# Optimization experiments

Hardware: AMD Instinct MI355X
Metric: run time of the kernel (lower is better)

## Reference

```python
import jax, jax.numpy as jnp
import numpy as np

B, S, D = 2, 2048, 2048
H, KV, HD = 32, 8, 64          # n_heads, n_kv_heads, head_dim
REP = H // KV                  # 4
THETA = 10000.0


def _rotate_half(u):
    h = u.shape[-1] // 2
    return jnp.concatenate([-u[..., h:], u[..., :h]], axis=-1)


def setup_inputs() -> dict:
    key = jax.random.key(0)
    ks = jax.random.split(key, 5)
    x = jax.random.normal(ks[0], (B, S, D), dtype=jnp.float32)
    Wq = jax.random.normal(ks[1], (D, H * HD), dtype=jnp.float32) * 0.02
    Wk = jax.random.normal(ks[2], (D, KV * HD), dtype=jnp.float32) * 0.02
    Wv = jax.random.normal(ks[3], (D, KV * HD), dtype=jnp.float32) * 0.02
    Wo = jax.random.normal(ks[4], (H * HD, D), dtype=jnp.float32) * 0.02
    return {"x": x, "Wq": Wq, "Wk": Wk, "Wv": Wv, "Wo": Wo}


def reference(x, Wq, Wk, Wv, Wo):
    b, s, d = x.shape
    # QKV projections (nn.Linear, no bias)
    q = (x @ Wq).reshape(b, s, H, HD).transpose(0, 2, 1, 3)   # [B,H,S,HD]
    k = (x @ Wk).reshape(b, s, KV, HD).transpose(0, 2, 1, 3)  # [B,KV,S,HD]
    v = (x @ Wv).reshape(b, s, KV, HD).transpose(0, 2, 1, 3)  # [B,KV,S,HD]

    # RoPE (position_offset = 0)
    inv_freq = 1.0 / (THETA ** (jnp.arange(0, HD, 2, dtype=jnp.float32) / HD))
    freqs = jnp.outer(jnp.arange(s, dtype=jnp.float32), inv_freq)  # [S,HD/2]
    emb = jnp.concatenate([freqs, freqs], axis=-1)                  # [S,HD]
    cos, sin = jnp.cos(emb), jnp.sin(emb)
    q = q * cos + _rotate_half(q) * sin
    k = k * cos + _rotate_half(k) * sin

    # Grouped attention: avoid materializing repeated KV tensors.
    qg = q.reshape(b, KV, REP, s, HD)                               # [B,KV,REP,S,HD]
    scale = 1.0 / np.sqrt(HD)
    scores = jnp.einsum('bgrqd,bgkd->bgrqk', qg, k) * scale         # [B,KV,REP,S,S]
    causal = jnp.tril(jnp.ones((s, s), dtype=bool))
    scores = jnp.where(causal, scores, jnp.finfo(jnp.float32).min)
    probs = jax.nn.softmax(scores.astype(jnp.float32), axis=-1).astype(q.dtype)
    out = jnp.einsum('bgrqk,bgkd->bgrqd', probs, v)                 # [B,KV,REP,S,HD]
    out = out.reshape(b, H, s, HD).transpose(0, 2, 1, 3).reshape(b, s, H * HD)
    return out @ Wo                                                  # [B,S,D]
```

## Files before the change

### kernel.cpp

```cpp
#include <hip/hip_runtime.h>
#include <math.h>

typedef __bf16 bf16_t;
typedef bf16_t bf16x8 __attribute__((ext_vector_type(8)));
typedef bf16_t bf16x4 __attribute__((ext_vector_type(4)));
typedef float floatx4 __attribute__((ext_vector_type(4)));
typedef short short4v __attribute__((ext_vector_type(4)));

#define MFMA16(a, b, c) __builtin_amdgcn_mfma_f32_16x16x32_bf16((a), (b), (c), 0, 0, 0)

#if __has_builtin(__builtin_amdgcn_exp2f)
#define PEXP(x) __builtin_amdgcn_exp2f(x)
#define SCORE_SCALE (0.125f * 1.4426950408889634f)
#else
#define PEXP(x) __expf(x)
#define SCORE_SCALE 0.125f
#endif

#if __has_builtin(__builtin_amdgcn_mfma_f32_16x16x16bf16_1k)
#define HAVE_MFMA_K16 1
__device__ __forceinline__ floatx4 mfma_k16(bf16x4 a, bf16x4 b, floatx4 c)
{
    union { bf16x4 v; short4v s; } ua, ub;
    ua.v = a; ub.v = b;
    return __builtin_amdgcn_mfma_f32_16x16x16bf16_1k(ua.s, ub.s, c, 0, 0, 0);
}
#endif

union PU { unsigned u[2]; bf16x4 v; };
union BU { unsigned u[4]; bf16x8 v; };

__device__ __forceinline__ void gld16(const void* g, void* lds)
{
    __builtin_amdgcn_global_load_lds(
        reinterpret_cast<const __attribute__((address_space(1))) void*>(
            reinterpret_cast<uintptr_t>(g)),
        reinterpret_cast<__attribute__((address_space(3))) void*>(
            (unsigned int)reinterpret_cast<uintptr_t>(lds)),
        16, 0, 0);
}

template <int RND>
__device__ __forceinline__ void stageT(
    const bf16_t* __restrict__ g, int K, int r0, int k0,
    bf16_t* lds, int tid, int wave)
{
    #pragma unroll
    for (int i = 0; i < RND; ++i) {
        int c = i * 512 + tid, r = c >> 3, s = c & 7;
        gld16(g + (size_t)(r0 + r) * K + k0 + ((s ^ (r & 7)) << 3),
              lds + (size_t)(i * 512 + wave * 64) * 8);
    }
}

template <typename TC, int BN>
__device__ __forceinline__ void gemm256_body(
    const bf16_t* __restrict__ A, const bf16_t* __restrict__ Bt,
    TC* __restrict__ C, int row0, int col0, int N, int K, bf16_t* smem)
{
    constexpr int NT = BN / 64;
    constexpr int NH = NT / 2;
    constexpr int RB = BN / 64;

    const int tid  = threadIdx.x;
    const int wave = tid >> 6, lane = tid & 63;
    const int quad = lane >> 4, l16 = lane & 15;
    const int wm = (wave >> 2) * 128;
    const int wn = (wave & 3) * (BN / 4);

    bf16_t* As0 = smem;
    bf16_t* As1 = smem + 256 * 64;
    bf16_t* Bs0 = smem + 2 * 256 * 64;
    bf16_t* Bs1 = Bs0 + BN * 64;

    const int ntile = K >> 6;

    floatx4 acc[8][NT] = {};

    stageT<4>(A, K, row0, 0, As0, tid, wave);
    stageT<RB>(Bt, K, col0, 0, Bs0, tid, wave);
    stageT<4>(A, K, row0, 64, As1, tid, wave);

    #pragma unroll 1
    for (int u = 0; u < ntile; ++u) {
        const int d = u & 1;
        bf16_t* Asd = d ? As1 : As0;
        bf16_t* Bsd = d ? Bs1 : Bs0;

        if (u + 1 < ntile)
            __asm__ volatile("s_waitcnt vmcnt(4)" ::: "memory");
        else
            __asm__ volatile("s_waitcnt vmcnt(0)" ::: "memory");
        __builtin_amdgcn_s_barrier();
        __asm__ volatile("" ::: "memory");

        if (u + 1 < ntile)
            stageT<RB>(Bt, K, col0, (u + 1) << 6, d ? Bs0 : Bs1, tid, wave);

        bf16x8 af[8][2], bfr[NH][2];
        #pragma unroll
        for (int mt = 0; mt < 8; ++mt)
            #pragma unroll
            for (int kh = 0; kh < 2; ++kh) {
                int ar = wm + mt * 16 + l16;
                af[mt][kh] = *(const bf16x8*)&Asd[ar * 64 +
                    (((kh * 4 + quad) ^ (ar & 7)) << 3)];
            }
        #pragma unroll
        for (int j = 0; j < NH; ++j)
            #pragma unroll
            for (int kh = 0; kh < 2; ++kh) {
                int br = wn + j * 16 + l16;
                bfr[j][kh] = *(const bf16x8*)&Bsd[br * 64 +
                    (((kh * 4 + quad) ^ (br & 7)) << 3)];
            }

        __builtin_amdgcn_s_setprio(1);
        #pragma unroll
        for (int kh = 0; kh < 2; ++kh)
            #pragma unroll
            for (int mt = 0; mt < 8; ++mt)
                #pragma unroll
                for (int j = 0; j < NH; ++j)
                    acc[mt][j] = MFMA16(af[mt][kh], bfr[j][kh], acc[mt][j]);
        __builtin_amdgcn_s_setprio(0);

        __asm__ volatile("s_waitcnt lgkmcnt(0)" ::: "memory");
        __builtin_amdgcn_s_barrier();
        __asm__ volatile("" ::: "memory");

        if (u + 2 < ntile)
            stageT<4>(A, K, row0, (u + 2) << 6, Asd, tid, wave);

        bf16x8 bf1[NH][2];
        #pragma unroll
        for (int j = 0; j < NH; ++j)
            #pragma unroll
            for (int kh = 0; kh < 2; ++kh) {
                int br = wn + (NH + j) * 16 + l16;
                bf1[j][kh] = *(const bf16x8*)&Bsd[br * 64 +
                    (((kh * 4 + quad) ^ (br & 7)) << 3)];
            }

        __builtin_amdgcn_s_setprio(1);
        #pragma unroll
        for (int kh = 0; kh < 2; ++kh)
            #pragma unroll
            for (int mt = 0; mt < 8; ++mt)
                #pragma unroll
                for (int j = 0; j < NH; ++j)
                    acc[mt][NH + j] = MFMA16(af[mt][kh], bf1[j][kh],
                                             acc[mt][NH + j]);
        __builtin_amdgcn_s_setprio(0);
    }

    #pragma unroll
    for (int mt = 0; mt < 8; ++mt)
        #pragma unroll
        for (int nt = 0; nt < NT; ++nt)
            #pragma unroll
            for (int r = 0; r < 4; ++r)
                C[(size_t)(row0 + wm + mt * 16 + quad * 4 + r) * N
                  + col0 + wn + nt * 16 + l16] = (TC)acc[mt][nt][r];
}

__global__ __launch_bounds__(512, 2) void gemm256_qkv(
    const bf16_t* __restrict__ A, const bf16_t* __restrict__ BtQ,
    const bf16_t* __restrict__ BtK, const bf16_t* __restrict__ BtV,
    bf16_t* __restrict__ CQ, bf16_t* __restrict__ CK, bf16_t* __restrict__ CV)
{
    extern __shared__ __align__(16) bf16_t smem[];
    const int x = blockIdx.x;
    const bf16_t* Bt; bf16_t* C; int N, col0;
    if (x < 8)       { Bt = BtQ; C = CQ; N = 2048; col0 = x * 256; }
    else if (x < 10) { Bt = BtK; C = CK; N = 512;  col0 = (x - 8) * 256; }
    else             { Bt = BtV; C = CV; N = 512;  col0 = (x - 10) * 256; }
    gemm256_body<bf16_t, 256>(A, Bt, C, blockIdx.y * 256, col0, N, 2048, smem);
}

__global__ __launch_bounds__(512, 2) void gemm256_out(
    const bf16_t* __restrict__ A, const bf16_t* __restrict__ Bt,
    float* __restrict__ C)
{
    extern __shared__ __align__(16) bf16_t smem[];
    gemm256_body<float, 128>(A, Bt, C, blockIdx.y * 256, blockIdx.x * 128,
                             2048, 2048, smem);
}

__device__ __forceinline__ void transpose_body(
    const float* __restrict__ W, bf16_t* __restrict__ Wt, int K, int N,
    int bx, int by, float (*t)[33], int tid)
{
    int tx = tid & 31, ty = tid >> 5;
    #pragma unroll
    for (int i = 0; i < 32; i += 8)
        t[ty + i][tx] = W[(size_t)(by + ty + i) * N + bx + tx];
    __syncthreads();
    #pragma unroll
    for (int i = 0; i < 32; i += 8)
        Wt[(size_t)(bx + ty + i) * K + by + tx] = (bf16_t)t[tx][ty + i];
}

__global__ __launch_bounds__(256) void prep_all(
    const float* __restrict__ x, const float* __restrict__ Wq,
    const float* __restrict__ Wk, const float* __restrict__ Wv,
    bf16_t* __restrict__ xb, bf16_t* __restrict__ WqT,
    bf16_t* __restrict__ WkT, bf16_t* __restrict__ WvT)
{
    __shared__ float t[32][33];
    const int blk = blockIdx.x, tid = threadIdx.x;
    if (blk < 8192) {
        int i = blk * 256 + tid;
        float4 f = ((const float4*)x)[i];
        bf16x4 v = {(bf16_t)f.x, (bf16_t)f.y, (bf16_t)f.z, (bf16_t)f.w};
        ((bf16x4*)xb)[i] = v;
    } else if (blk < 12288) {
        int r = blk - 8192;
        transpose_body(Wq, WqT, 2048, 2048, (r & 63) * 32, (r >> 6) * 32, t, tid);
    } else if (blk < 13312) {
        int r = blk - 12288;
        transpose_body(Wk, WkT, 2048, 512, (r & 15) * 32, (r >> 4) * 32, t, tid);
    } else {
        int r = blk - 13312;
        transpose_body(Wv, WvT, 2048, 512, (r & 15) * 32, (r >> 4) * 32, t, tid);
    }
}

__global__ __launch_bounds__(256) void mid_all(
    bf16_t* __restrict__ Kw, const bf16_t* __restrict__ Vw,
    bf16_t* __restrict__ VtG, const float* __restrict__ Wo,
    bf16_t* __restrict__ WoT)
{
    __shared__ float tf[32][33];
    __shared__ bf16_t tb[32][34];
    const int blk = blockIdx.x, tid = threadIdx.x;
    if (blk < 4096) {
        int idx = blk * 256 + tid;
        int i   = idx & 31;
        int h   = (idx >> 5) & 7;
        int row = idx >> 8;
        int pos = row & 2047;
        float invf = powf(10000.0f, -(float)i / 32.0f);
        float sv, cv;
        sincosf((float)pos * invf, &sv, &cv);
        size_t base = (size_t)row * 512 + (size_t)h * 64 + i;
        float a  = (float)Kw[base];
        float b2 = (float)Kw[base + 32];
        Kw[base]      = (bf16_t)(a * cv - b2 * sv);
        Kw[base + 32] = (bf16_t)(b2 * cv + a * sv);
    } else if (blk < 6144) {
        int r  = blk - 4096;
        int bz = r >> 10, r2 = r & 1023;
        int bx = (r2 & 15) * 32, by = (r2 >> 4) * 32;
        int tx = tid & 31, ty = tid >> 5;
        #pragma unroll
        for (int i = 0; i < 32; i += 8)
            tb[ty + i][tx] = Vw[((size_t)bz * 2048 + by + ty + i) * 512 + bx + tx];
        __syncthreads();
        #pragma unroll
        for (int i = 0; i < 32; i += 8)
            VtG[((size_t)bz * 512 + bx + ty + i) * 2048 + by + tx] = tb[tx][ty + i];
    } else {
        int r = blk - 6144;
        transpose_body(Wo, WoT, 2048, 2048, (r & 63) * 32, (r >> 6) * 32, tf, tid);
    }
}

__global__ __launch_bounds__(256, 2) void gqa_attn(
    const bf16_t* __restrict__ Q, const bf16_t* __restrict__ Kc,
    const bf16_t* __restrict__ Vt, bf16_t* __restrict__ AO)
{
    __shared__ alignas(16) bf16_t Ks[2][64 * 64];
    __shared__ alignas(16) bf16_t Vs[2][64 * 64];

    const int bid = blockIdx.x;
    const int l   = (bid & 7) * 64 + (bid >> 3);
    const int g   = l >> 6;
    const int b   = (l >> 5) & 1;
    const int x   = l & 31;

    const int tid  = threadIdx.x;
    const int wave = tid >> 6, lane = tid & 63;
    const int quad = lane >> 4, l16 = lane & 15;
    const int h = g * 4 + wave;

    #pragma unroll 1
    for (int t = 0; t < 2; ++t) {
        const int qt = t ? x : (63 - x);
        const int q0 = qt * 32;
        int qb[2];
        qb[0] = q0;
        qb[1] = q0 + 16;

        bf16x8 qf[2][2];
        #pragma unroll
        for (int mt = 0; mt < 2; ++mt) {
            int qrow = qb[mt] + l16;
            const bf16_t* qp = Q + (size_t)(b * 2048 + qrow) * 2048 + h * 64 + quad * 8;
            bf16x8 lo = *(const bf16x8*)qp;
            bf16x8 hi = *(const bf16x8*)(qp + 32);
            #pragma unroll
            for (int j = 0; j < 8; ++j) {
                int d = quad * 8 + j;
                float invf = powf(10000.0f, -(float)d / 32.0f);
                float sv, cv;
                sincosf((float)qrow * invf, &sv, &cv);
                float a = (float)lo[j], c2 = (float)hi[j];
                qf[mt][0][j] = (bf16_t)((a * cv - c2 * sv) * SCORE_SCALE);
                qf[mt][1][j] = (bf16_t)((c2 * cv + a * sv) * SCORE_SCALE);
            }
        }

        floatx4 o[2][4] = {};
        floatx4 ls4[2] = {};

        const int ktmax = qt >> 1;

        __asm__ volatile("s_waitcnt lgkmcnt(0)" ::: "memory");
        __builtin_amdgcn_s_barrier();
        #pragma unroll
        for (int i = 0; i < 2; ++i) {
            int c = i * 256 + tid;
            int r = c >> 3, s = c & 7;
            int sw = (s ^ (r & 7)) << 3;
            gld16(Kc + (size_t)(b * 2048 + r) * 512 + g * 64 + sw,
                  &Ks[0][(i * 256 + wave * 64) * 8]);
            gld16(Vt + (size_t)(b * 512 + g * 64 + r) * 2048 + sw,
                  &Vs[0][(i * 256 + wave * 64) * 8]);
        }

        #pragma unroll 1
        for (int kt = 0; kt <= ktmax; ++kt) {
            const int cur = kt & 1;
            if (kt < ktmax) {
                const int kn = kt + 1;
                #pragma unroll
                for (int i = 0; i < 2; ++i) {
                    int c = i * 256 + tid;
                    int r = c >> 3, s = c & 7;
                    int sw = (s ^ (r & 7)) << 3;
                    gld16(Kc + (size_t)(b * 2048 + kn * 64 + r) * 512 + g * 64 + sw,
                          &Ks[cur ^ 1][(i * 256 + wave * 64) * 8]);
                    gld16(Vt + (size_t)(b * 512 + g * 64 + r) * 2048 + kn * 64 + sw,
                          &Vs[cur ^ 1][(i * 256 + wave * 64) * 8]);
                }
                __asm__ volatile("s_waitcnt vmcnt(4)" ::: "memory");
            } else {
                __asm__ volatile("s_waitcnt vmcnt(0)" ::: "memory");
            }
            __builtin_amdgcn_s_barrier();

            floatx4 st[2][4] = {};
            __builtin_amdgcn_s_setprio(1);
            #pragma unroll
            for (int nt = 0; nt < 4; ++nt) {
                int kr = nt * 16 + l16;
                bf16x8 kf0 = *(const bf16x8*)&Ks[cur][kr * 64 + ((quad ^ (kr & 7)) << 3)];
                bf16x8 kf1 = *(const bf16x8*)&Ks[cur][kr * 64 + (((4 + quad) ^ (kr & 7)) << 3)];
                st[0][nt] = MFMA16(kf0, qf[0][0], st[0][nt]);
                st[0][nt] = MFMA16(kf1, qf[0][1], st[0][nt]);
                st[1][nt] = MFMA16(kf0, qf[1][0], st[1][nt]);
                st[1][nt] = MFMA16(kf1, qf[1][1], st[1][nt]);
            }
            __builtin_amdgcn_s_setprio(0);

            PU pk[2][4];
            const bool diag = (kt == ktmax);
            #pragma unroll
            for (int mt = 0; mt < 2; ++mt) {
                const int qa = qb[mt] + l16;
                #pragma unroll
                for (int nt = 0; nt < 4; ++nt) {
                    float pv[4];
                    #pragma unroll
                    for (int r = 0; r < 4; ++r) {
                        float e = PEXP(st[mt][nt][r]);
                        if (diag) {
                            int ka = kt * 64 + nt * 16 + quad * 4 + r;
                            if (ka > qa) e = 0.f;
                        }
                        ls4[mt][r] += e;
                        pv[r] = e;
                    }
                    pk[mt][nt].v = bf16x4{(bf16_t)pv[0], (bf16_t)pv[1],
                                          (bf16_t)pv[2], (bf16_t)pv[3]};
                }
            }

#ifdef HAVE_MFMA_K16
            __builtin_amdgcn_s_setprio(1);
            #pragma unroll
            for (int nt = 0; nt < 4; ++nt)
                #pragma unroll
                for (int dt = 0; dt < 4; ++dt) {
                    int vr = dt * 16 + l16;
                    int slot = ((nt << 1) | (quad >> 1)) ^ (vr & 7);
                    bf16x4 va = *(const bf16x4*)&Vs[cur][vr * 64 + (slot << 3)
                                                         + ((quad & 1) << 2)];
                    o[0][dt] = mfma_k16(va, pk[0][nt].v, o[0][dt]);
                    o[1][dt] = mfma_k16(va, pk[1][nt].v, o[1][dt]);
                }
            __builtin_amdgcn_s_setprio(0);
#else
            #pragma unroll
            for (int H = 0; H < 2; ++H) {
                BU bfv[2];
                #pragma unroll
                for (int mt = 0; mt < 2; ++mt) {
                    #pragma unroll
                    for (int j = 0; j < 4; ++j) {
                        int srcl = (((quad & 1) << 1) + (j >> 1)) * 16 + l16;
                        unsigned a0 = (unsigned)__shfl((int)pk[mt][2 * H].u[j & 1], srcl, 64);
                        unsigned a1 = (unsigned)__shfl((int)pk[mt][2 * H + 1].u[j & 1], srcl, 64);
                        bfv[mt].u[j] = (quad >> 1) ? a1 : a0;
                    }
                }
                #pragma unroll
                for (int dt = 0; dt < 4; ++dt) {
                    int vr = dt * 16 + l16;
                    bf16x8 va = *(const bf16x8*)&Vs[cur][vr * 64
                                  + ((((H << 2) | quad) ^ (vr & 7)) << 3)];
                    o[0][dt] = MFMA16(va, bfv[0].v, o[0][dt]);
                    o[1][dt] = MFMA16(va, bfv[1].v, o[1][dt]);
                }
            }
#endif
            __asm__ volatile("s_waitcnt lgkmcnt(0)" ::: "memory");
            __builtin_amdgcn_s_barrier();
        }

        #pragma unroll
        for (int mt = 0; mt < 2; ++mt) {
            float l2 = ls4[mt][0] + ls4[mt][1] + ls4[mt][2] + ls4[mt][3];
            l2 += __shfl_xor(l2, 16, 64);
            l2 += __shfl_xor(l2, 32, 64);
            float rc = 1.0f / l2;
            #pragma unroll
            for (int dt = 0; dt < 4; ++dt) {
                bf16x4 ov = {(bf16_t)(o[mt][dt][0] * rc), (bf16_t)(o[mt][dt][1] * rc),
                             (bf16_t)(o[mt][dt][2] * rc), (bf16_t)(o[mt][dt][3] * rc)};
                *(bf16x4*)&AO[(size_t)(b * 2048 + qb[mt] + l16) * 2048
                              + h * 64 + dt * 16 + quad * 4] = ov;
            }
        }
    }
}

extern "C" void kernel_launch(void* const* d_in, const int* in_sizes, int n_in,
                              void* d_out, int out_size, void* d_ws, size_t ws_size,
                              hipStream_t stream)
{
    const float* x  = (const float*)d_in[0];
    const float* Wq = (const float*)d_in[1];
    const float* Wk = (const float*)d_in[2];
    const float* Wv = (const float*)d_in[3];
    const float* Wo = (const float*)d_in[4];
    float* out = (float*)d_out;

    const size_t MB = 1024 * 1024;
    char* ws = (char*)d_ws;
    bf16_t* xb_AO = (bf16_t*)(ws);
    bf16_t* WqoT  = (bf16_t*)(ws + 16 * MB);
    bf16_t* WkT   = (bf16_t*)(ws + 24 * MB);
    bf16_t* WvT   = (bf16_t*)(ws + 26 * MB);
    bf16_t* Qw    = (bf16_t*)(ws + 28 * MB);
    bf16_t* Kw    = (bf16_t*)(ws + 44 * MB);
    bf16_t* Vw    = (bf16_t*)(ws + 48 * MB);
    bf16_t* VtG   = (bf16_t*)(ws + 52 * MB);

    static bool s_attr = false;
    if (!s_attr) {
        hipFuncSetAttribute(reinterpret_cast<const void*>(gemm256_qkv),
                            hipFuncAttributeMaxDynamicSharedMemorySize, 131072);
        hipFuncSetAttribute(reinterpret_cast<const void*>(gemm256_out),
                            hipFuncAttributeMaxDynamicSharedMemorySize, 98304);
        s_attr = true;
    }

    prep_all<<<14336, 256, 0, stream>>>(x, Wq, Wk, Wv, xb_AO, WqoT, WkT, WvT);

    gemm256_qkv<<<dim3(12, 16), 512, 131072, stream>>>(
        xb_AO, WqoT, WkT, WvT, Qw, Kw, Vw);

    mid_all<<<10240, 256, 0, stream>>>(Kw, Vw, VtG, Wo, WqoT);

    gqa_attn<<<dim3(512), 256, 0, stream>>>(Qw, Kw, VtG, xb_AO);

    gemm256_out<<<dim3(16, 16), 512, 98304, stream>>>(xb_AO, WqoT, out);
}
```

Baseline: 289.2 us.

## Fuse K RoPE into QKV GEMM epilogue, compute V transposed, drop mid kernel

Applies RoPE to K in the QKV GEMM epilogue instead of a separate pass. V is now produced already transposed by swapping the GEMM operands (WvT times x), so the transpose pass disappears. The Wo transpose moves into extra blocks of the attention launch, which removes the mid_all kernel and one launch plus its global round trips. The trade-offs are extra sincos work in the GEMM epilogue, a V layout with a 4096 stride, and transpose blocks competing with attention blocks for the GPU.

New measurement: 336.4 us. 1.16x slower.

```diff
diff --git a/kernel.cpp b/kernel.cpp
--- a/kernel.cpp
+++ b/kernel.cpp
@@ -53,7 +53,7 @@
     }
 }
 
-template <typename TC, int BN>
+template <typename TC, int BN, bool ROPE>
 __device__ __forceinline__ void gemm256_body(
     const bf16_t* __restrict__ A, const bf16_t* __restrict__ Bt,
     TC* __restrict__ C, int row0, int col0, int N, int K, bf16_t* smem)
@@ -154,6 +154,29 @@
         __builtin_amdgcn_s_setprio(0);
     }
 
+    if constexpr (ROPE) {
+        float invf[2];
+        #pragma unroll
+        for (int nt = 0; nt < 2; ++nt)
+            invf[nt] = powf(10000.0f, -(float)(nt * 16 + l16) / 32.0f);
+        #pragma unroll
+        for (int mt = 0; mt < 8; ++mt)
+            #pragma unroll
+            for (int r = 0; r < 4; ++r) {
+                int row = row0 + wm + mt * 16 + quad * 4 + r;
+                float pos = (float)(row & 2047);
+                #pragma unroll
+                for (int nt = 0; nt < 2; ++nt) {
+                    float sv, cv;
+                    sincosf(pos * invf[nt], &sv, &cv);
+                    float a  = acc[mt][nt][r];
+                    float b2 = acc[mt][nt + 2][r];
+                    acc[mt][nt][r]     = a * cv - b2 * sv;
+                    acc[mt][nt + 2][r] = b2 * cv + a * sv;
+                }
+            }
+    }
+
     #pragma unroll
     for (int mt = 0; mt < 8; ++mt)
         #pragma unroll
@@ -166,16 +189,21 @@
 
 __global__ __launch_bounds__(512, 2) void gemm256_qkv(
     const bf16_t* __restrict__ A, const bf16_t* __restrict__ BtQ,
-    const bf16_t* __restrict__ BtK, const bf16_t* __restrict__ BtV,
-    bf16_t* __restrict__ CQ, bf16_t* __restrict__ CK, bf16_t* __restrict__ CV)
+    const bf16_t* __restrict__ BtK, const bf16_t* __restrict__ WvT,
+    bf16_t* __restrict__ CQ, bf16_t* __restrict__ CK, bf16_t* __restrict__ CVt)
 {
     extern __shared__ __align__(16) bf16_t smem[];
     const int x = blockIdx.x;
-    const bf16_t* Bt; bf16_t* C; int N, col0;
-    if (x < 8)       { Bt = BtQ; C = CQ; N = 2048; col0 = x * 256; }
-    else if (x < 10) { Bt = BtK; C = CK; N = 512;  col0 = (x - 8) * 256; }
-    else             { Bt = BtV; C = CV; N = 512;  col0 = (x - 10) * 256; }
-    gemm256_body<bf16_t, 256>(A, Bt, C, blockIdx.y * 256, col0, N, 2048, smem);
+    if (x < 8) {
+        gemm256_body<bf16_t, 256, false>(A, BtQ, CQ, blockIdx.y * 256,
+                                         x * 256, 2048, 2048, smem);
+    } else if (x < 10) {
+        gemm256_body<bf16_t, 256, true>(A, BtK, CK, blockIdx.y * 256,
+                                        (x - 8) * 256, 512, 2048, smem);
+    } else {
+        gemm256_body<bf16_t, 256, false>(WvT, A, CVt, (x - 10) * 256,
+                                         blockIdx.y * 256, 4096, 2048, smem);
+    }
 }
 
 __global__ __launch_bounds__(512, 2) void gemm256_out(
@@ -183,8 +211,8 @@
     float* __restrict__ C)
 {
     extern __shared__ __align__(16) bf16_t smem[];
-    gemm256_body<float, 128>(A, Bt, C, blockIdx.y * 256, blockIdx.x * 128,
-                             2048, 2048, smem);
+    gemm256_body<float, 128, false>(A, Bt, C, blockIdx.y * 256,
+                                    blockIdx.x * 128, 2048, 2048, smem);
 }
 
 __device__ __forceinline__ void transpose_body(
@@ -226,54 +254,23 @@
     }
 }
 
-__global__ __launch_bounds__(256) void mid_all(
-    bf16_t* __restrict__ Kw, const bf16_t* __restrict__ Vw,
-    bf16_t* __restrict__ VtG, const float* __restrict__ Wo,
-    bf16_t* __restrict__ WoT)
-{
-    __shared__ float tf[32][33];
-    __shared__ bf16_t tb[32][34];
-    const int blk = blockIdx.x, tid = threadIdx.x;
-    if (blk < 4096) {
-        int idx = blk * 256 + tid;
-        int i   = idx & 31;
-        int h   = (idx >> 5) & 7;
-        int row = idx >> 8;
-        int pos = row & 2047;
-        float invf = powf(10000.0f, -(float)i / 32.0f);
-        float sv, cv;
-        sincosf((float)pos * invf, &sv, &cv);
-        size_t base = (size_t)row * 512 + (size_t)h * 64 + i;
-        float a  = (float)Kw[base];
-        float b2 = (float)Kw[base + 32];
-        Kw[base]      = (bf16_t)(a * cv - b2 * sv);
-        Kw[base + 32] = (bf16_t)(b2 * cv + a * sv);
-    } else if (blk < 6144) {
-        int r  = blk - 4096;
-        int bz = r >> 10, r2 = r & 1023;
-        int bx = (r2 & 15) * 32, by = (r2 >> 4) * 32;
-        int tx = tid & 31, ty = tid >> 5;
-        #pragma unroll
-        for (int i = 0; i < 32; i += 8)
-            tb[ty + i][tx] = Vw[((size_t)bz * 2048 + by + ty + i) * 512 + bx + tx];
-        __syncthreads();
-        #pragma unroll
-        for (int i = 0; i < 32; i += 8)
-            VtG[((size_t)bz * 512 + bx + ty + i) * 2048 + by + tx] = tb[tx][ty + i];
-    } else {
-        int r = blk - 6144;
-        transpose_body(Wo, WoT, 2048, 2048, (r & 63) * 32, (r >> 6) * 32, tf, tid);
-    }
-}
-
 __global__ __launch_bounds__(256, 2) void gqa_attn(
     const bf16_t* __restrict__ Q, const bf16_t* __restrict__ Kc,
-    const bf16_t* __restrict__ Vt, bf16_t* __restrict__ AO)
+    const bf16_t* __restrict__ Vt, bf16_t* __restrict__ AO,
+    const float* __restrict__ Wo, bf16_t* __restrict__ WoT)
 {
     __shared__ alignas(16) bf16_t Ks[2][64 * 64];
     __shared__ alignas(16) bf16_t Vs[2][64 * 64];
 
     const int bid = blockIdx.x;
+    if (bid >= 512) {
+        int r = bid - 512;
+        float (*tf)[33] = reinterpret_cast<float(*)[33]>(&Ks[0][0]);
+        transpose_body(Wo, WoT, 2048, 2048, (r & 63) * 32, (r >> 6) * 32,
+                       tf, threadIdx.x);
+        return;
+    }
+
     const int l   = (bid & 7) * 64 + (bid >> 3);
     const int g   = l >> 6;
     const int b   = (l >> 5) & 1;
@@ -325,7 +322,7 @@
             int sw = (s ^ (r & 7)) << 3;
             gld16(Kc + (size_t)(b * 2048 + r) * 512 + g * 64 + sw,
                   &Ks[0][(i * 256 + wave * 64) * 8]);
-            gld16(Vt + (size_t)(b * 512 + g * 64 + r) * 2048 + sw,
+            gld16(Vt + (size_t)(g * 64 + r) * 4096 + b * 2048 + sw,
                   &Vs[0][(i * 256 + wave * 64) * 8]);
         }
 
@@ -341,7 +338,7 @@
                     int sw = (s ^ (r & 7)) << 3;
                     gld16(Kc + (size_t)(b * 2048 + kn * 64 + r) * 512 + g * 64 + sw,
                           &Ks[cur ^ 1][(i * 256 + wave * 64) * 8]);
-                    gld16(Vt + (size_t)(b * 512 + g * 64 + r) * 2048 + kn * 64 + sw,
+                    gld16(Vt + (size_t)(g * 64 + r) * 4096 + b * 2048 + kn * 64 + sw,
                           &Vs[cur ^ 1][(i * 256 + wave * 64) * 8]);
                 }
                 __asm__ volatile("s_waitcnt vmcnt(4)" ::: "memory");
@@ -465,8 +462,7 @@
     bf16_t* WvT   = (bf16_t*)(ws + 26 * MB);
     bf16_t* Qw    = (bf16_t*)(ws + 28 * MB);
     bf16_t* Kw    = (bf16_t*)(ws + 44 * MB);
-    bf16_t* Vw    = (bf16_t*)(ws + 48 * MB);
-    bf16_t* VtG   = (bf16_t*)(ws + 52 * MB);
+    bf16_t* VtG   = (bf16_t*)(ws + 48 * MB);
 
     static bool s_attr = false;
     if (!s_attr) {
@@ -480,11 +476,9 @@
     prep_all<<<14336, 256, 0, stream>>>(x, Wq, Wk, Wv, xb_AO, WqoT, WkT, WvT);
 
     gemm256_qkv<<<dim3(12, 16), 512, 131072, stream>>>(
-        xb_AO, WqoT, WkT, WvT, Qw, Kw, Vw);
-
-    mid_all<<<10240, 256, 0, stream>>>(Kw, Vw, VtG, Wo, WqoT);
-
-    gqa_attn<<<dim3(512), 256, 0, stream>>>(Qw, Kw, VtG, xb_AO);
+        xb_AO, WqoT, WkT, WvT, Qw, Kw, VtG);
+
+    gqa_attn<<<dim3(4608), 256, 0, stream>>>(Qw, Kw, VtG, xb_AO, Wo, WqoT);
 
     gemm256_out<<<dim3(16, 16), 512, 98304, stream>>>(xb_AO, WqoT, out);
 }
```
